# Performance work log

Hardware: AMD Instinct MI355X
Metric: run time of the kernel (lower is better)

The kernel has to match this reference:

```python
import jax, jax.numpy as jnp
import numpy as np

B, T, DM, DFE, DH, DRH = 32, 2048, 128, 64, 64, 64
E, NF, NSF, TOPK = 8, 16, 64, 2
LN_EPS = 1e-5


def setup_inputs() -> dict:
    key = jax.random.key(0)
    ks = jax.random.split(key, 18)
    s = 0.05
    # base expert i owns columns [16*i, 16*i+16); scale=2 -> expert e uses base e//2
    expert_idx = jnp.asarray(np.stack([np.arange(NF) + NF * (e // 2) for e in range(E)]), dtype=jnp.int32)  # [E,NF]
    stage_idx = jnp.arange(NSF, dtype=jnp.int32)  # stage uses all 64 columns
    return {
        'hidden': jax.random.normal(ks[0], (B, T, DM), jnp.float32),
        'feat': jax.random.normal(ks[1], (B, T, NSF), jnp.float32),
        'ln_g': jnp.ones((DM,), jnp.float32),
        'ln_b': jnp.zeros((DM,), jnp.float32),
        'Wp': jax.random.normal(ks[2], (NSF, DFE), jnp.float32) * s,
        'bp': jnp.zeros((DFE,), jnp.float32),
        'Wr1': jax.random.normal(ks[3], (DM + DFE, DRH), jnp.float32) * s,
        'br1': jnp.zeros((DRH,), jnp.float32),
        'Wr2': jax.random.normal(ks[4], (DRH, E), jnp.float32) * s,
        'br2': jnp.zeros((E,), jnp.float32),
        'Wf': jax.random.normal(ks[5], (E, NF, DFE), jnp.float32) * s,
        'bf': jnp.zeros((E, DFE), jnp.float32),
        'We1h': jax.random.normal(ks[6], (E, DM, DH), jnp.float32) * s,
        'We1f': jax.random.normal(ks[7], (E, DFE, DH), jnp.float32) * s,
        'be1': jnp.zeros((E, DH), jnp.float32),
        'We2': jax.random.normal(ks[8], (E, DH, DM), jnp.float32) * s,
        'be2': jnp.zeros((E, DM), jnp.float32),
        'alpha': jnp.asarray(1.0, jnp.float32),
        'item_seq_len': jax.random.randint(ks[9], (B,), 1, T + 1),
        'expert_idx': expert_idx,
        'stage_idx': stage_idx,
    }


def _layernorm(x, g, b):
    mu = jnp.mean(x, -1, keepdims=True)
    v = jnp.mean(jnp.square(x - mu), -1, keepdims=True)
    return (x - mu) * jax.lax.rsqrt(v + LN_EPS) * g + b


def reference(hidden, feat, ln_g, ln_b, Wp, bp, Wr1, br1, Wr2, br2,
              Wf, bf, We1h, We1f, be1, We2, be2, alpha,
              item_seq_len, expert_idx, stage_idx):
    h = _layernorm(hidden, ln_g, ln_b)                         # [B,T,DM]  pre_ln
    femb = feat[..., stage_idx] @ Wp + bp                      # [B,T,DFE] stage feature projection
    # --- token router: MLP -> softmax(temp=1) -> top-k renormalized gates ---
    rin = jnp.concatenate([h, femb], -1)                       # [B,T,DM+DFE]
    logits = jax.nn.relu(rin @ Wr1 + br1) @ Wr2 + br2          # [B,T,E]
    probs = jax.nn.softmax(logits, axis=-1)
    topv, topi = jax.lax.top_k(probs, TOPK)                    # [B,T,K]
    topv = topv / jnp.sum(topv, -1, keepdims=True)
    gates = jnp.sum(jax.nn.one_hot(topi, E, dtype=probs.dtype) * topv[..., None], axis=-2)  # [B,T,E]
    valid = jnp.arange(T)[None, :] < item_seq_len[:, None]     # [B,T]
    gates = gates * valid[..., None].astype(gates.dtype)
    # --- experts: per-expert feature gather + 2-layer GELU MLP (hidden + feat inputs) ---
    ef = feat[:, :, expert_idx]                                # [B,T,E,NF] gather
    x = jnp.einsum('btef,efd->bted', ef, Wf) + bf              # [B,T,E,DFE]
    h1 = jax.nn.gelu(jnp.einsum('btd,edo->bteo', h, We1h)
                     + jnp.einsum('bted,edo->bteo', x, We1f) + be1, approximate=False)
    eo = jnp.einsum('bteo,eod->bted', h1, We2) + be2           # [B,T,E,DM]
    moe = jnp.einsum('bte,bted->btd', gates, eo)               # weighted combine
    next_hidden = hidden + alpha * moe                         # residual, alpha_scale=1, dropout=0
    return next_hidden, gates, probs
```

## Files before the change

### kernel.cpp

```cpp
#include <hip/hip_runtime.h>
#include <hip/hip_bf16.h>


typedef unsigned short u16;
typedef __attribute__((ext_vector_type(8))) short bfrag;
typedef __attribute__((ext_vector_type(8))) u16 u16x8;
typedef __attribute__((ext_vector_type(4))) float facc;
typedef __attribute__((ext_vector_type(4))) float f32x4;

#define NTOK 65536
#define CAP 65536

#define OFF_CNT   ((size_t)0)
#define OFF_SEGM  ((size_t)256)
#define OFF_LTOK  ((size_t)512)
#define OFF_SMAPG (OFF_LTOK + (size_t)8*CAP*4)
#define OFF_HWS   (OFF_SMAPG + (size_t)NTOK*8)
#define OFF_EOTOK (OFF_HWS + (size_t)NTOK*128*2)
#define OFF_W1T   (OFF_EOTOK + (size_t)NTOK*2*128*2)
#define OFF_W2T   (OFF_W1T + 196608)
#define OFF_B1P   (OFF_W2T + 131072)
#define OFF_WPR   (OFF_B1P + 2048)
#define OFF_BR1P  (OFF_WPR + 16384)

__device__ __forceinline__ u16 f2bf(float f) {
  union { __hip_bfloat16 h; u16 u; } cv;
  cv.h = __float2bfloat16(f);
  return cv.u;
}
__device__ __forceinline__ float bf2f(u16 u) {
  return __uint_as_float(((unsigned)u) << 16);
}

__global__ __launch_bounds__(256)
void k0_pre(const float* __restrict__ Wp, const float* __restrict__ bp,
            const float* __restrict__ Wr1, const float* __restrict__ br1,
            const float* __restrict__ Wf, const float* __restrict__ bfv,
            const float* __restrict__ We1h, const float* __restrict__ We1f,
            const float* __restrict__ be1, const float* __restrict__ We2,
            float* __restrict__ Wpr, float* __restrict__ br1p,
            u16* __restrict__ w1t, u16* __restrict__ w2t, float* __restrict__ b1p)
{
  int j = blockIdx.x * 256 + threadIdx.x;
  if (j < 4096) {
    int i = j >> 6, o = j & 63;
    float s = 0.f;
    for (int k = 0; k < 64; ++k) s += Wp[i*64+k] * Wr1[(128+k)*64 + o];
    Wpr[i*64+o] = s;
  } else if (j < 4160) {
    int o = j - 4096;
    float s = br1[o];
    for (int k = 0; k < 64; ++k) s += bp[k] * Wr1[(128+k)*64 + o];
    br1p[o] = s;
  } else if (j < 4160 + 98304) {
    int idx = j - 4160;
    int e = idx / 12288; int rem = idx % 12288;
    int jj = rem / 192; int k = rem % 192;
    float v = 0.f;
    if (k < 128) v = We1h[(e*128 + k)*64 + jj];
    else if (k < 144) {
      int i = k - 128; float s = 0.f;
      for (int d = 0; d < 64; ++d) s += Wf[(e*16+i)*64 + d] * We1f[(e*64+d)*64 + jj];
      v = s;
    }
    size_t byte = (size_t)(e*64 + jj)*384 + ((2*k) ^ ((jj & 7) << 4));
    *(u16*)((char*)w1t + byte) = f2bf(v);
  } else if (j < 4160 + 98304 + 65536) {
    int idx = j - 4160 - 98304;
    int e = idx / 8192; int rem = idx % 8192;
    int d = rem / 64; int k = rem & 63;
    float v = We2[(e*64 + k)*128 + d];
    size_t byte = (size_t)(e*128 + d)*128 + ((2*k) ^ ((d & 7) << 4));
    *(u16*)((char*)w2t + byte) = f2bf(v);
  } else if (j < 4160 + 98304 + 65536 + 512) {
    int idx = j - 4160 - 98304 - 65536;
    int e = idx >> 6, o = idx & 63;
    float s = be1[e*64 + o];
    for (int d = 0; d < 64; ++d) s += bfv[e*64 + d] * We1f[(e*64+d)*64 + o];
    b1p[e*64 + o] = s;
  }
}

__global__ __launch_bounds__(256, 4)
void k1_router(const float* __restrict__ hidden, const float* __restrict__ feat,
               const float* __restrict__ ln_g, const float* __restrict__ ln_b,
               const float* __restrict__ Wr1, const float* __restrict__ Wr2,
               const float* __restrict__ br2, const int* __restrict__ seqlen,
               const int* __restrict__ sidx_g,
               const float* __restrict__ Wpr, const float* __restrict__ br1p,
               float* __restrict__ outG, float* __restrict__ outP,
               u16* __restrict__ hws, int* __restrict__ cnt,
               int* __restrict__ listTok, float* __restrict__ smapG)
{
  __shared__ float At[64*64];
  __shared__ float Wc[64*64];
  __shared__ float sW2[512];
  __shared__ float sb1[64], sg[128], sb[128], sbr2[8];
  __shared__ int ssidx[64];
  __shared__ int lcnt[8], lbase[8];
  __shared__ int ltok[8][64];
  __shared__ float tg[64][2];

  int tid = threadIdx.x;
  for (int i = tid; i < 512; i += 256) sW2[i] = Wr2[i];
  if (tid < 128) sg[tid] = ln_g[tid]; else sb[tid-128] = ln_b[tid-128];
  if (tid < 64) { sb1[tid] = br1p[tid]; ssidx[tid] = sidx_g[tid]; }
  if (tid >= 64 && tid < 72) sbr2[tid-64] = br2[tid-64];
  if (tid >= 72 && tid < 80) lcnt[tid-72] = 0;
  __syncthreads();

  int tok = tid >> 2, q = tid & 3;
  int t = blockIdx.x * 64 + tok;

  f32x4 x[8];
  #pragma unroll
  for (int i = 0; i < 8; ++i) x[i] = *(const f32x4*)(hidden + (size_t)t*128 + q*32 + i*4);
  float s = 0.f;
  #pragma unroll
  for (int i = 0; i < 8; ++i) { s += x[i][0] + x[i][1]; s += x[i][2] + x[i][3]; }
  s += __shfl_xor(s, 1, 64); s += __shfl_xor(s, 2, 64);
  float mu = s * (1.f/128.f);
  float v = 0.f;
  #pragma unroll
  for (int i = 0; i < 8; ++i) {
    #pragma unroll
    for (int j = 0; j < 4; ++j) { float d = x[i][j] - mu; v = fmaf(d, d, v); }
  }
  v += __shfl_xor(v, 1, 64); v += __shfl_xor(v, 2, 64);
  float rs = rsqrtf(v * (1.f/128.f) + 1e-5f);
  #pragma unroll
  for (int i = 0; i < 8; ++i) {
    #pragma unroll
    for (int j = 0; j < 4; ++j) {
      int c = q*32 + i*4 + j;
      x[i][j] = (x[i][j] - mu) * rs * sg[c] + sb[c];
    }
  }
  #pragma unroll
  for (int m = 0; m < 4; ++m) {
    u16x8 o;
    #pragma unroll
    for (int j = 0; j < 4; ++j) { o[j] = f2bf(x[2*m][j]); o[4+j] = f2bf(x[2*m+1][j]); }
    *(u16x8*)(hws + (size_t)t*128 + q*32 + m*8) = o;
  }
  float fv[16];
  #pragma unroll
  for (int i = 0; i < 16; ++i) fv[i] = feat[(size_t)t*64 + ssidx[q*16 + i]];

  float acc[4][4];
  #pragma unroll
  for (int i = 0; i < 4; ++i)
    #pragma unroll
    for (int p = 0; p < 4; ++p) acc[i][p] = 0.f;

  int tb = tid >> 4;
  int ob = (tid & 15) * 4;

  #pragma unroll 1
  for (int c = 0; c < 3; ++c) {
    __syncthreads();
    if (c < 2) {
      if ((c == 0) ? (q < 2) : (q >= 2)) {
        int kbase = (c == 0) ? q*32 : (q-2)*32;
        #pragma unroll
        for (int i = 0; i < 8; ++i)
          #pragma unroll
          for (int j = 0; j < 4; ++j) {
            int kr = kbase + i*4 + j;
            int byte = (kr << 8) + ((((tok >> 2) ^ ((kr >> 2) & 15)) << 4) | ((tok & 3) << 2));
            *(float*)((char*)At + byte) = x[i][j];
          }
      }
    } else {
      #pragma unroll
      for (int i = 0; i < 16; ++i) {
        int kr = q*16 + i;
        int byte = (kr << 8) + ((((tok >> 2) ^ ((kr >> 2) & 15)) << 4) | ((tok & 3) << 2));
        *(float*)((char*)At + byte) = fv[i];
      }
    }
    const float* wsrc = (c == 0) ? Wr1 : (c == 1) ? (Wr1 + 4096) : Wpr;
    for (int i = tid; i < 1024; i += 256) ((f32x4*)Wc)[i] = ((const f32x4*)wsrc)[i];
    __syncthreads();
    #pragma unroll 4
    for (int k = 0; k < 64; ++k) {
      f32x4 a4 = *(const f32x4*)((const char*)At + (k << 8) + ((tb ^ ((k >> 2) & 15)) << 4));
      f32x4 b4 = *(const f32x4*)(Wc + k*64 + ob);
      #pragma unroll
      for (int i = 0; i < 4; ++i)
        #pragma unroll
        for (int p = 0; p < 4; ++p)
          acc[i][p] = fmaf(a4[i], b4[p], acc[i][p]);
    }
  }

  float w2r[4][8];
  #pragma unroll
  for (int p = 0; p < 4; ++p)
    #pragma unroll
    for (int e = 0; e < 8; ++e) w2r[p][e] = sW2[(ob + p)*8 + e];
  float b1r[4];
  #pragma unroll
  for (int p = 0; p < 4; ++p) b1r[p] = sb1[ob + p];

  int j16 = tid & 15;
  #pragma unroll 1
  for (int ti = 0; ti < 4; ++ti) {
    float lo[8];
    #pragma unroll
    for (int e = 0; e < 8; ++e) lo[e] = 0.f;
    #pragma unroll
    for (int p = 0; p < 4; ++p) {
      float z = fmaxf(acc[ti][p] + b1r[p], 0.f);
      #pragma unroll
      for (int e = 0; e < 8; ++e) lo[e] = fmaf(z, w2r[p][e], lo[e]);
    }
    #pragma unroll
    for (int m = 1; m < 16; m <<= 1) {
      #pragma unroll
      for (int e = 0; e < 8; ++e) lo[e] += __shfl_xor(lo[e], m, 64);
    }
    #pragma unroll
    for (int e = 0; e < 8; ++e) lo[e] += sbr2[e];

    int tloc = tb*4 + ti;
    int tt = blockIdx.x*64 + tloc;
    float mx = lo[0];
    #pragma unroll
    for (int e = 1; e < 8; ++e) mx = fmaxf(mx, lo[e]);
    float ex[8]; float ss = 0.f;
    #pragma unroll
    for (int e = 0; e < 8; ++e) { ex[e] = __expf(lo[e] - mx); ss += ex[e]; }
    float inv = 1.f / ss;
    float p[8];
    #pragma unroll
    for (int e = 0; e < 8; ++e) p[e] = ex[e] * inv;
    float p1 = p[0]; int i1 = 0;
    #pragma unroll
    for (int e = 1; e < 8; ++e) { bool tk2 = p[e] > p1; p1 = tk2 ? p[e] : p1; i1 = tk2 ? e : i1; }
    float p2 = -1.f; int i2 = 0;
    #pragma unroll
    for (int e = 0; e < 8; ++e) { bool tk2 = (e != i1) && (p[e] > p2); p2 = tk2 ? p[e] : p2; i2 = tk2 ? e : i2; }
    bool valid = (tt & 2047) < seqlen[tt >> 11];
    float gden = 1.f / (p1 + p2);
    float g1 = p1 * gden, g2 = p2 * gden;
    float pv = p[0];
    #pragma unroll
    for (int e = 1; e < 8; ++e) pv = (j16 == e) ? p[e] : pv;
    if (j16 < 8) outP[(size_t)tt*8 + j16] = pv;
    float gv = (j16 == i1) ? g1 : ((j16 == i2) ? g2 : 0.f);
    if (!valid) gv = 0.f;
    if (j16 < 8) outG[(size_t)tt*8 + j16] = gv;
    if (j16 == 0) {
      if (valid) {
        int lp = atomicAdd(&lcnt[i1], 1); ltok[i1][lp] = (tt << 1);
        lp = atomicAdd(&lcnt[i2], 1);     ltok[i2][lp] = (tt << 1) | 1;
        tg[tloc][0] = g1; tg[tloc][1] = g2;
      } else {
        tg[tloc][0] = 0.f; tg[tloc][1] = 0.f;
      }
    }
  }

  __syncthreads();
  if (tid < 8) lbase[tid] = atomicAdd(&cnt[tid], lcnt[tid]);
  __syncthreads();
  #pragma unroll 1
  for (int e = 0; e < 8; ++e) {
    int ncnt = lcnt[e];
    if (tid < ncnt) listTok[(size_t)e*CAP + lbase[e] + tid] = ltok[e][tid];
  }
  if (tid < 64) {
    float2 g; g.x = tg[tid][0]; g.y = tg[tid][1];
    ((float2*)smapG)[blockIdx.x*64 + tid] = g;
  }
}

__global__ void k1b_prefix(const int* __restrict__ cnt, int* __restrict__ segm)
{
  if (threadIdx.x == 0 && blockIdx.x == 0) {
    int s = 0;
    #pragma unroll
    for (int e = 0; e < 8; ++e) { segm[e] = s; s += (cnt[e] + 63) >> 6; }
    segm[8] = s;
  }
}

__global__ __launch_bounds__(256)
void k2_experts(const float* __restrict__ feat, const u16* __restrict__ hws,
                const u16* __restrict__ w1t, const u16* __restrict__ w2t,
                const float* __restrict__ b1p, const float* __restrict__ be2,
                const int* __restrict__ eidx_g, const int* __restrict__ cnt,
                const int* __restrict__ segm, const int* __restrict__ listTok,
                u16* __restrict__ eoTok)
{
  __shared__ u16 Xs[64*192];
  __shared__ u16 W1s[64*192];
  __shared__ u16 W2s[128*64];
  __shared__ u16 H1s[64*64];
  __shared__ float b1s[64], be2s[128];
  __shared__ int sent[64];
  __shared__ int seidx[16];
  __shared__ int snr;

  int b = blockIdx.x;
  if (b >= segm[8]) return;
  int e = 0;
  #pragma unroll
  for (int i = 1; i < 8; ++i) if (b >= segm[i]) e = i;
  int row0 = (b - segm[e]) << 6;
  int n = cnt[e];
  int nr = n - row0; if (nr > 64) nr = 64;
  int tid = threadIdx.x;
  if (tid == 0) snr = nr;

  if (tid < 64) {
    int ent = 0;
    if (tid < nr) ent = listTok[(size_t)e*CAP + row0 + tid];
    sent[tid] = ent;
    b1s[tid] = b1p[e*64 + tid];
  }
  if (tid >= 64 && tid < 192) be2s[tid - 64] = be2[e*128 + tid - 64];
  if (tid >= 192 && tid < 208) seidx[tid-192] = eidx_g[e*16 + tid - 192];
  {
    const u16x8* s1 = (const u16x8*)(w1t + e*64*192);
    u16x8* d1 = (u16x8*)W1s;
    for (int i = tid; i < 1536; i += 256) d1[i] = s1[i];
    const u16x8* s2 = (const u16x8*)(w2t + e*128*64);
    u16x8* d2 = (u16x8*)W2s;
    for (int i = tid; i < 1024; i += 256) d2[i] = s2[i];
  }
  __syncthreads();
  for (int c = tid; c < 1024; c += 256) {
    int r = c >> 4, p = c & 15;
    u16x8 v = *(const u16x8*)(hws + (size_t)(sent[r] >> 1)*128 + p*8);
    *(u16x8*)((char*)Xs + r*384 + ((p*16) ^ ((r & 7) << 4))) = v;
  }
  if (tid < 128) {
    int r = tid >> 1, hf = tid & 1;
    int tk = sent[r] >> 1;
    u16x8 ov;
    #pragma unroll
    for (int p = 0; p < 8; ++p) ov[p] = f2bf(feat[(size_t)tk*64 + seidx[hf*8 + p]]);
    *(u16x8*)((char*)Xs + r*384 + ((256 + hf*16) ^ ((r & 7) << 4))) = ov;
    u16x8 zv = {0,0,0,0,0,0,0,0};
    *(u16x8*)((char*)Xs + r*384 + ((288 + hf*16) ^ ((r & 7) << 4))) = zv;
  }
  __syncthreads();

  int w = tid >> 6, lane = tid & 63;
  int la = lane & 15, lg = lane >> 4;
  int wm = (w >> 1) * 32, wn = (w & 1) * 32;

  facc acc[2][2];
  #pragma unroll
  for (int a = 0; a < 2; ++a)
    #pragma unroll
    for (int b2 = 0; b2 < 2; ++b2) { facc z = {0.f,0.f,0.f,0.f}; acc[a][b2] = z; }
  #pragma unroll
  for (int kc = 0; kc < 5; ++kc) {
    int kb = kc*64 + lg*16;
    bfrag af[2], bf2[2];
    #pragma unroll
    for (int mi = 0; mi < 2; ++mi) {
      int r = wm + mi*16 + la;
      af[mi] = *(const bfrag*)((const char*)Xs + r*384 + (kb ^ ((r & 7) << 4)));
    }
    #pragma unroll
    for (int ni = 0; ni < 2; ++ni) {
      int r = wn + ni*16 + la;
      bf2[ni] = *(const bfrag*)((const char*)W1s + r*384 + (kb ^ ((r & 7) << 4)));
    }
    #pragma unroll
    for (int mi = 0; mi < 2; ++mi)
      #pragma unroll
      for (int ni = 0; ni < 2; ++ni)
        acc[mi][ni] = __builtin_amdgcn_mfma_f32_16x16x32_bf16(af[mi], bf2[ni], acc[mi][ni], 0, 0, 0);
  }
  #pragma unroll
  for (int mi = 0; mi < 2; ++mi)
    #pragma unroll
    for (int ni = 0; ni < 2; ++ni)
      #pragma unroll
      for (int rg = 0; rg < 4; ++rg) {
        int r = wm + mi*16 + lg*4 + rg;
        int c = wn + ni*16 + la;
        float z = acc[mi][ni][rg] + b1s[c];
        float gl = 0.5f * z * (1.f + erff(z * 0.70710678118f));
        *(u16*)((char*)H1s + r*128 + ((2*c) ^ ((r & 7) << 4))) = f2bf(gl);
      }
  __syncthreads();

  facc acc2[2][4];
  #pragma unroll
  for (int a = 0; a < 2; ++a)
    #pragma unroll
    for (int b2 = 0; b2 < 4; ++b2) { facc z = {0.f,0.f,0.f,0.f}; acc2[a][b2] = z; }
  int wn2 = (w & 1) * 64;
  #pragma unroll
  for (int kc = 0; kc < 2; ++kc) {
    int kb = kc*64 + lg*16;
    bfrag af[2], bf2[4];
    #pragma unroll
    for (int mi = 0; mi < 2; ++mi) {
      int r = wm + mi*16 + la;
      af[mi] = *(const bfrag*)((const char*)H1s + r*128 + (kb ^ ((r & 7) << 4)));
    }
    #pragma unroll
    for (int ni = 0; ni < 4; ++ni) {
      int r = wn2 + ni*16 + la;
      bf2[ni] = *(const bfrag*)((const char*)W2s + r*128 + (kb ^ ((r & 7) << 4)));
    }
    #pragma unroll
    for (int mi = 0; mi < 2; ++mi)
      #pragma unroll
      for (int ni = 0; ni < 4; ++ni)
        acc2[mi][ni] = __builtin_amdgcn_mfma_f32_16x16x32_bf16(af[mi], bf2[ni], acc2[mi][ni], 0, 0, 0);
  }
  #pragma unroll
  for (int mi = 0; mi < 2; ++mi)
    #pragma unroll
    for (int ni = 0; ni < 4; ++ni)
      #pragma unroll
      for (int rg = 0; rg < 4; ++rg) {
        int r = wm + mi*16 + lg*4 + rg;
        int c = wn2 + ni*16 + la;
        if (r < snr) {
          float v = acc2[mi][ni][rg] + be2s[c];
          eoTok[(size_t)sent[r]*128 + c] = f2bf(v);
        }
      }
}

__global__ __launch_bounds__(256)
void k3_combine(const float* __restrict__ hidden, const float* __restrict__ smapG,
                const u16* __restrict__ eoTok, const float* __restrict__ alphap,
                float* __restrict__ outN)
{
  int tid = threadIdx.x;
  int tok = tid >> 2, q = tid & 3;
  int t = blockIdx.x*64 + tok;
  float2 g = ((const float2*)smapG)[t];
  float a = alphap[0];
  float ag0 = a * g.x, ag1 = a * g.y;
  const f32x4* hp = (const f32x4*)(hidden + (size_t)t*128 + q*32);
  f32x4* op = (f32x4*)(outN + (size_t)t*128 + q*32);
  const u16x8* e0 = (const u16x8*)(eoTok + ((size_t)t*2)*128 + q*32);
  const u16x8* e1 = (const u16x8*)(eoTok + ((size_t)t*2 + 1)*128 + q*32);
  #pragma unroll
  for (int i = 0; i < 4; ++i) {
    f32x4 r0 = hp[2*i], r1 = hp[2*i+1];
    if (g.x != 0.f) {
      u16x8 x0 = e0[i];
      #pragma unroll
      for (int j = 0; j < 4; ++j) { r0[j] = fmaf(ag0, bf2f(x0[j]), r0[j]); r1[j] = fmaf(ag0, bf2f(x0[4+j]), r1[j]); }
    }
    if (g.y != 0.f) {
      u16x8 x1 = e1[i];
      #pragma unroll
      for (int j = 0; j < 4; ++j) { r0[j] = fmaf(ag1, bf2f(x1[j]), r0[j]); r1[j] = fmaf(ag1, bf2f(x1[4+j]), r1[j]); }
    }
    op[2*i] = r0; op[2*i+1] = r1;
  }
}

extern "C" void kernel_launch(void* const* d_in, const int* in_sizes, int n_in,
                              void* d_out, int out_size, void* d_ws, size_t ws_size,
                              hipStream_t stream) {
  const float* hidden = (const float*)d_in[0];
  const float* feat   = (const float*)d_in[1];
  const float* ln_g   = (const float*)d_in[2];
  const float* ln_b   = (const float*)d_in[3];
  const float* Wp     = (const float*)d_in[4];
  const float* bp     = (const float*)d_in[5];
  const float* Wr1    = (const float*)d_in[6];
  const float* br1    = (const float*)d_in[7];
  const float* Wr2    = (const float*)d_in[8];
  const float* br2    = (const float*)d_in[9];
  const float* Wf     = (const float*)d_in[10];
  const float* bfv    = (const float*)d_in[11];
  const float* We1h   = (const float*)d_in[12];
  const float* We1f   = (const float*)d_in[13];
  const float* be1    = (const float*)d_in[14];
  const float* We2    = (const float*)d_in[15];
  const float* be2    = (const float*)d_in[16];
  const float* alpha  = (const float*)d_in[17];
  const int* seqlen   = (const int*)d_in[18];
  const int* eidx     = (const int*)d_in[19];
  const int* sidx     = (const int*)d_in[20];

  char* ws = (char*)d_ws;
  int*   cnt      = (int*)(ws + OFF_CNT);
  int*   segm     = (int*)(ws + OFF_SEGM);
  int*   listTok  = (int*)(ws + OFF_LTOK);
  float* smapG    = (float*)(ws + OFF_SMAPG);
  u16*   hws      = (u16*)(ws + OFF_HWS);
  u16*   eoTok    = (u16*)(ws + OFF_EOTOK);
  u16*   w1t      = (u16*)(ws + OFF_W1T);
  u16*   w2t      = (u16*)(ws + OFF_W2T);
  float* b1p      = (float*)(ws + OFF_B1P);
  float* Wpr      = (float*)(ws + OFF_WPR);
  float* br1p     = (float*)(ws + OFF_BR1P);

  float* outN = (float*)d_out;
  float* outG = outN + (size_t)NTOK * 128;
  float* outP = outG + (size_t)NTOK * 8;

  hipMemsetAsync(ws + OFF_CNT, 0, 256, stream);
  k0_pre<<<659, 256, 0, stream>>>(Wp, bp, Wr1, br1, Wf, bfv, We1h, We1f, be1, We2,
                                  Wpr, br1p, w1t, w2t, b1p);
  k1_router<<<1024, 256, 0, stream>>>(hidden, feat, ln_g, ln_b, Wr1, Wr2, br2, seqlen,
                                      sidx, Wpr, br1p, outG, outP, hws, cnt,
                                      listTok, smapG);
  k1b_prefix<<<1, 64, 0, stream>>>(cnt, segm);
  k2_experts<<<2056, 256, 0, stream>>>(feat, hws, w1t, w2t, b1p, be2, eidx,
                                       cnt, segm, listTok, eoTok);
  k3_combine<<<1024, 256, 0, stream>>>(hidden, smapG, eoTok, alpha, outN);
}
```

Baseline: 129.8 us.

## Drop prefix kernel, read expert weights from global, prefetch router weights

The separate single-thread prefix kernel is removed, and each expert block now computes its segment from the counts inline. The expert kernel stops staging the W1/W2 weights into shared memory. It reads MFMA B-fragments straight from global/L2, uses padded unswizzled LDS rows for X and H1, and gives each wave a 16-row M tile. The router kernel register-prefetches the next weight chunk while computing the current one and uses a different LDS swizzle. Together these cut one launch and LDS traffic and occupancy pressure, at the cost of more global/L2 weight reads per block.

```diff
diff --git a/kernel.cpp b/kernel.cpp
--- a/kernel.cpp
+++ b/kernel.cpp
@@ -12,13 +12,12 @@
 #define CAP 65536
 
 #define OFF_CNT   ((size_t)0)
-#define OFF_SEGM  ((size_t)256)
 #define OFF_LTOK  ((size_t)512)
 #define OFF_SMAPG (OFF_LTOK + (size_t)8*CAP*4)
 #define OFF_HWS   (OFF_SMAPG + (size_t)NTOK*8)
 #define OFF_EOTOK (OFF_HWS + (size_t)NTOK*128*2)
 #define OFF_W1T   (OFF_EOTOK + (size_t)NTOK*2*128*2)
-#define OFF_W2T   (OFF_W1T + 196608)
+#define OFF_W2T   (OFF_W1T + 163840)
 #define OFF_B1P   (OFF_W2T + 131072)
 #define OFF_WPR   (OFF_B1P + 2048)
 #define OFF_BR1P  (OFF_WPR + 16384)
@@ -52,10 +51,10 @@
     float s = br1[o];
     for (int k = 0; k < 64; ++k) s += bp[k] * Wr1[(128+k)*64 + o];
     br1p[o] = s;
-  } else if (j < 4160 + 98304) {
+  } else if (j < 4160 + 81920) {
     int idx = j - 4160;
-    int e = idx / 12288; int rem = idx % 12288;
-    int jj = rem / 192; int k = rem % 192;
+    int e = idx / 10240; int rem = idx % 10240;
+    int jj = rem / 160; int k = rem % 160;
     float v = 0.f;
     if (k < 128) v = We1h[(e*128 + k)*64 + jj];
     else if (k < 144) {
@@ -63,17 +62,14 @@
       for (int d = 0; d < 64; ++d) s += Wf[(e*16+i)*64 + d] * We1f[(e*64+d)*64 + jj];
       v = s;
     }
-    size_t byte = (size_t)(e*64 + jj)*384 + ((2*k) ^ ((jj & 7) << 4));
-    *(u16*)((char*)w1t + byte) = f2bf(v);
-  } else if (j < 4160 + 98304 + 65536) {
-    int idx = j - 4160 - 98304;
+    w1t[(size_t)(e*64 + jj)*160 + k] = f2bf(v);
+  } else if (j < 4160 + 81920 + 65536) {
+    int idx = j - 4160 - 81920;
     int e = idx / 8192; int rem = idx % 8192;
     int d = rem / 64; int k = rem & 63;
-    float v = We2[(e*64 + k)*128 + d];
-    size_t byte = (size_t)(e*128 + d)*128 + ((2*k) ^ ((d & 7) << 4));
-    *(u16*)((char*)w2t + byte) = f2bf(v);
-  } else if (j < 4160 + 98304 + 65536 + 512) {
-    int idx = j - 4160 - 98304 - 65536;
+    w2t[(size_t)(e*128 + d)*64 + k] = f2bf(We2[(e*64 + k)*128 + d]);
+  } else if (j < 4160 + 81920 + 65536 + 512) {
+    int idx = j - 4160 - 81920 - 65536;
     int e = idx >> 6, o = idx & 63;
     float s = be1[e*64 + o];
     for (int d = 0; d < 64; ++d) s += bfv[e*64 + d] * We1f[(e*64+d)*64 + o];
@@ -102,6 +98,11 @@
   __shared__ float tg[64][2];
 
   int tid = threadIdx.x;
+
+  f32x4 wpf[4];
+  #pragma unroll
+  for (int u = 0; u < 4; ++u) wpf[u] = ((const f32x4*)Wr1)[u*256 + tid];
+
   for (int i = tid; i < 512; i += 256) sW2[i] = Wr2[i];
   if (tid < 128) sg[tid] = ln_g[tid]; else sb[tid-128] = ln_b[tid-128];
   if (tid < 64) { sb1[tid] = br1p[tid]; ssidx[tid] = sidx_g[tid]; }
@@ -158,7 +159,6 @@
 
   #pragma unroll 1
   for (int c = 0; c < 3; ++c) {
-    __syncthreads();
     if (c < 2) {
       if ((c == 0) ? (q < 2) : (q >= 2)) {
         int kbase = (c == 0) ? q*32 : (q-2)*32;
@@ -167,24 +167,30 @@
           #pragma unroll
           for (int j = 0; j < 4; ++j) {
             int kr = kbase + i*4 + j;
-            int byte = (kr << 8) + ((((tok >> 2) ^ ((kr >> 2) & 15)) << 4) | ((tok & 3) << 2));
-            *(float*)((char*)At + byte) = x[i][j];
+            int slot = ((tok >> 2) ^ (kr & 15) ^ (kr >> 4)) & 15;
+            *(float*)((char*)At + (kr << 8) + (slot << 4) + ((tok & 3) << 2)) = x[i][j];
           }
       }
     } else {
       #pragma unroll
       for (int i = 0; i < 16; ++i) {
         int kr = q*16 + i;
-        int byte = (kr << 8) + ((((tok >> 2) ^ ((kr >> 2) & 15)) << 4) | ((tok & 3) << 2));
-        *(float*)((char*)At + byte) = fv[i];
+        int slot = ((tok >> 2) ^ (kr & 15) ^ (kr >> 4)) & 15;
+        *(float*)((char*)At + (kr << 8) + (slot << 4) + ((tok & 3) << 2)) = fv[i];
       }
     }
-    const float* wsrc = (c == 0) ? Wr1 : (c == 1) ? (Wr1 + 4096) : Wpr;
-    for (int i = tid; i < 1024; i += 256) ((f32x4*)Wc)[i] = ((const f32x4*)wsrc)[i];
+    #pragma unroll
+    for (int u = 0; u < 4; ++u) ((f32x4*)Wc)[u*256 + tid] = wpf[u];
     __syncthreads();
+    if (c < 2) {
+      const f32x4* nsrc = (c == 0) ? (const f32x4*)(Wr1 + 4096) : (const f32x4*)Wpr;
+      #pragma unroll
+      for (int u = 0; u < 4; ++u) wpf[u] = nsrc[u*256 + tid];
+    }
     #pragma unroll 4
     for (int k = 0; k < 64; ++k) {
-      f32x4 a4 = *(const f32x4*)((const char*)At + (k << 8) + ((tb ^ ((k >> 2) & 15)) << 4));
+      int slot = (tb ^ (k & 15) ^ (k >> 4)) & 15;
+      f32x4 a4 = *(const f32x4*)((const char*)At + (k << 8) + (slot << 4));
       f32x4 b4 = *(const f32x4*)(Wc + k*64 + ob);
       #pragma unroll
       for (int i = 0; i < 4; ++i)
@@ -192,6 +198,7 @@
         for (int p = 0; p < 4; ++p)
           acc[i][p] = fmaf(a4[i], b4[p], acc[i][p]);
     }
+    __syncthreads();
   }
 
   float w2r[4][8];
@@ -276,65 +283,47 @@
   }
 }
 
-__global__ void k1b_prefix(const int* __restrict__ cnt, int* __restrict__ segm)
-{
-  if (threadIdx.x == 0 && blockIdx.x == 0) {
-    int s = 0;
-    #pragma unroll
-    for (int e = 0; e < 8; ++e) { segm[e] = s; s += (cnt[e] + 63) >> 6; }
-    segm[8] = s;
-  }
-}
-
 __global__ __launch_bounds__(256)
 void k2_experts(const float* __restrict__ feat, const u16* __restrict__ hws,
                 const u16* __restrict__ w1t, const u16* __restrict__ w2t,
                 const float* __restrict__ b1p, const float* __restrict__ be2,
                 const int* __restrict__ eidx_g, const int* __restrict__ cnt,
-                const int* __restrict__ segm, const int* __restrict__ listTok,
-                u16* __restrict__ eoTok)
+                const int* __restrict__ listTok, u16* __restrict__ eoTok)
 {
-  __shared__ u16 Xs[64*192];
-  __shared__ u16 W1s[64*192];
-  __shared__ u16 W2s[128*64];
-  __shared__ u16 H1s[64*64];
+  __shared__ u16 Xs[64*168];
+  __shared__ u16 H1s[64*88];
   __shared__ float b1s[64], be2s[128];
   __shared__ int sent[64];
   __shared__ int seidx[16];
   __shared__ int snr;
 
-  int b = blockIdx.x;
-  if (b >= segm[8]) return;
-  int e = 0;
-  #pragma unroll
-  for (int i = 1; i < 8; ++i) if (b >= segm[i]) e = i;
-  int row0 = (b - segm[e]) << 6;
-  int n = cnt[e];
+  int b = blockIdx.x, tid = threadIdx.x;
+  int e = -1, row0 = 0, n = 0, accb = 0;
+  #pragma unroll
+  for (int i = 0; i < 8; ++i) {
+    int ci = cnt[i]; int ns = (ci + 63) >> 6;
+    if (e < 0 && b < accb + ns) { e = i; row0 = (b - accb) << 6; n = ci; }
+    accb += ns;
+  }
+  if (e < 0) return;
   int nr = n - row0; if (nr > 64) nr = 64;
-  int tid = threadIdx.x;
   if (tid == 0) snr = nr;
 
   if (tid < 64) {
-    int ent = 0;
-    if (tid < nr) ent = listTok[(size_t)e*CAP + row0 + tid];
+    int ent = (tid < nr) ? listTok[(size_t)e*CAP + row0 + tid] : 0;
     sent[tid] = ent;
     b1s[tid] = b1p[e*64 + tid];
-  }
-  if (tid >= 64 && tid < 192) be2s[tid - 64] = be2[e*128 + tid - 64];
-  if (tid >= 192 && tid < 208) seidx[tid-192] = eidx_g[e*16 + tid - 192];
-  {
-    const u16x8* s1 = (const u16x8*)(w1t + e*64*192);
-    u16x8* d1 = (u16x8*)W1s;
-    for (int i = tid; i < 1536; i += 256) d1[i] = s1[i];
-    const u16x8* s2 = (const u16x8*)(w2t + e*128*64);
-    u16x8* d2 = (u16x8*)W2s;
-    for (int i = tid; i < 1024; i += 256) d2[i] = s2[i];
-  }
-  __syncthreads();
-  for (int c = tid; c < 1024; c += 256) {
-    int r = c >> 4, p = c & 15;
-    u16x8 v = *(const u16x8*)(hws + (size_t)(sent[r] >> 1)*128 + p*8);
-    *(u16x8*)((char*)Xs + r*384 + ((p*16) ^ ((r & 7) << 4))) = v;
+  } else if (tid < 192) {
+    be2s[tid - 64] = be2[e*128 + tid - 64];
+  } else if (tid < 208) {
+    seidx[tid-192] = eidx_g[e*16 + tid - 192];
+  }
+  __syncthreads();
+
+  for (int c2 = tid; c2 < 1024; c2 += 256) {
+    int r = c2 >> 4, p = c2 & 15;
+    u16x8 vv = *(const u16x8*)(hws + (size_t)(sent[r] >> 1)*128 + p*8);
+    *(u16x8*)((char*)Xs + r*336 + p*16) = vv;
   }
   if (tid < 128) {
     int r = tid >> 1, hf = tid & 1;
@@ -342,94 +331,66 @@
     u16x8 ov;
     #pragma unroll
     for (int p = 0; p < 8; ++p) ov[p] = f2bf(feat[(size_t)tk*64 + seidx[hf*8 + p]]);
-    *(u16x8*)((char*)Xs + r*384 + ((256 + hf*16) ^ ((r & 7) << 4))) = ov;
+    *(u16x8*)((char*)Xs + r*336 + 256 + hf*16) = ov;
     u16x8 zv = {0,0,0,0,0,0,0,0};
-    *(u16x8*)((char*)Xs + r*384 + ((288 + hf*16) ^ ((r & 7) << 4))) = zv;
+    *(u16x8*)((char*)Xs + r*336 + 288 + hf*16) = zv;
   }
   __syncthreads();
 
   int w = tid >> 6, lane = tid & 63;
   int la = lane & 15, lg = lane >> 4;
-  int wm = (w >> 1) * 32, wn = (w & 1) * 32;
-
-  facc acc[2][2];
-  #pragma unroll
-  for (int a = 0; a < 2; ++a)
-    #pragma unroll
-    for (int b2 = 0; b2 < 2; ++b2) { facc z = {0.f,0.f,0.f,0.f}; acc[a][b2] = z; }
+  const u16* w1e = w1t + (size_t)e*64*160;
+  const u16* w2e = w2t + (size_t)e*128*64;
+
+  facc acc[4];
+  #pragma unroll
+  for (int ni = 0; ni < 4; ++ni) { facc z = {0.f,0.f,0.f,0.f}; acc[ni] = z; }
   #pragma unroll
   for (int kc = 0; kc < 5; ++kc) {
-    int kb = kc*64 + lg*16;
-    bfrag af[2], bf2[2];
-    #pragma unroll
-    for (int mi = 0; mi < 2; ++mi) {
-      int r = wm + mi*16 + la;
-      af[mi] = *(const bfrag*)((const char*)Xs + r*384 + (kb ^ ((r & 7) << 4)));
-    }
-    #pragma unroll
-    for (int ni = 0; ni < 2; ++ni) {
-      int r = wn + ni*16 + la;
-      bf2[ni] = *(const bfrag*)((const char*)W1s + r*384 + (kb ^ ((r & 7) << 4)));
-    }
-    #pragma unroll
-    for (int mi = 0; mi < 2; ++mi)
-      #pragma unroll
-      for (int ni = 0; ni < 2; ++ni)
-        acc[mi][ni] = __builtin_amdgcn_mfma_f32_16x16x32_bf16(af[mi], bf2[ni], acc[mi][ni], 0, 0, 0);
-  }
-  #pragma unroll
-  for (int mi = 0; mi < 2; ++mi)
-    #pragma unroll
-    for (int ni = 0; ni < 2; ++ni)
-      #pragma unroll
-      for (int rg = 0; rg < 4; ++rg) {
-        int r = wm + mi*16 + lg*4 + rg;
-        int c = wn + ni*16 + la;
-        float z = acc[mi][ni][rg] + b1s[c];
-        float gl = 0.5f * z * (1.f + erff(z * 0.70710678118f));
-        *(u16*)((char*)H1s + r*128 + ((2*c) ^ ((r & 7) << 4))) = f2bf(gl);
+    int r = w*16 + la;
+    bfrag af = *(const bfrag*)((const char*)Xs + r*336 + kc*64 + lg*16);
+    #pragma unroll
+    for (int ni = 0; ni < 4; ++ni) {
+      bfrag bf2 = *(const bfrag*)(w1e + (size_t)(ni*16 + la)*160 + kc*32 + lg*8);
+      acc[ni] = __builtin_amdgcn_mfma_f32_16x16x32_bf16(af, bf2, acc[ni], 0, 0, 0);
+    }
+  }
+  #pragma unroll
+  for (int ni = 0; ni < 4; ++ni)
+    #pragma unroll
+    for (int rg = 0; rg < 4; ++rg) {
+      int r = w*16 + lg*4 + rg;
+      int c = ni*16 + la;
+      float z = acc[ni][rg] + b1s[c];
+      float gl = 0.5f * z * (1.f + erff(z * 0.70710678118f));
+      *(u16*)((char*)H1s + r*176 + c*2) = f2bf(gl);
+    }
+  __syncthreads();
+
+  facc acc2[8];
+  #pragma unroll
+  for (int ni = 0; ni < 8; ++ni) { facc z = {0.f,0.f,0.f,0.f}; acc2[ni] = z; }
+  #pragma unroll
+  for (int kc = 0; kc < 2; ++kc) {
+    int r = w*16 + la;
+    bfrag af = *(const bfrag*)((const char*)H1s + r*176 + kc*64 + lg*16);
+    #pragma unroll
+    for (int ni = 0; ni < 8; ++ni) {
+      bfrag bf2 = *(const bfrag*)(w2e + (size_t)(ni*16 + la)*64 + kc*32 + lg*8);
+      acc2[ni] = __builtin_amdgcn_mfma_f32_16x16x32_bf16(af, bf2, acc2[ni], 0, 0, 0);
+    }
+  }
+  #pragma unroll
+  for (int ni = 0; ni < 8; ++ni)
+    #pragma unroll
+    for (int rg = 0; rg < 4; ++rg) {
+      int r = w*16 + lg*4 + rg;
+      int c = ni*16 + la;
+      if (r < snr) {
+        float vv = acc2[ni][rg] + be2s[c];
+        eoTok[(size_t)sent[r]*128 + c] = f2bf(vv);
       }
-  __syncthreads();
-
-  facc acc2[2][4];
-  #pragma unroll
-  for (int a = 0; a < 2; ++a)
-    #pragma unroll
-    for (int b2 = 0; b2 < 4; ++b2) { facc z = {0.f,0.f,0.f,0.f}; acc2[a][b2] = z; }
-  int wn2 = (w & 1) * 64;
-  #pragma unroll
-  for (int kc = 0; kc < 2; ++kc) {
-    int kb = kc*64 + lg*16;
-    bfrag af[2], bf2[4];
-    #pragma unroll
-    for (int mi = 0; mi < 2; ++mi) {
-      int r = wm + mi*16 + la;
-      af[mi] = *(const bfrag*)((const char*)H1s + r*128 + (kb ^ ((r & 7) << 4)));
-    }
-    #pragma unroll
-    for (int ni = 0; ni < 4; ++ni) {
-      int r = wn2 + ni*16 + la;
-      bf2[ni] = *(const bfrag*)((const char*)W2s + r*128 + (kb ^ ((r & 7) << 4)));
-    }
-    #pragma unroll
-    for (int mi = 0; mi < 2; ++mi)
-      #pragma unroll
-      for (int ni = 0; ni < 4; ++ni)
-        acc2[mi][ni] = __builtin_amdgcn_mfma_f32_16x16x32_bf16(af[mi], bf2[ni], acc2[mi][ni], 0, 0, 0);
-  }
-  #pragma unroll
-  for (int mi = 0; mi < 2; ++mi)
-    #pragma unroll
-    for (int ni = 0; ni < 4; ++ni)
-      #pragma unroll
-      for (int rg = 0; rg < 4; ++rg) {
-        int r = wm + mi*16 + lg*4 + rg;
-        int c = wn2 + ni*16 + la;
-        if (r < snr) {
-          float v = acc2[mi][ni][rg] + be2s[c];
-          eoTok[(size_t)sent[r]*128 + c] = f2bf(v);
-        }
-      }
+    }
 }
 
 __global__ __launch_bounds__(256)
@@ -491,7 +452,6 @@
 
   char* ws = (char*)d_ws;
   int*   cnt      = (int*)(ws + OFF_CNT);
-  int*   segm     = (int*)(ws + OFF_SEGM);
   int*   listTok  = (int*)(ws + OFF_LTOK);
   float* smapG    = (float*)(ws + OFF_SMAPG);
   u16*   hws      = (u16*)(ws + OFF_HWS);
@@ -507,13 +467,12 @@
   float* outP = outG + (size_t)NTOK * 8;
 
   hipMemsetAsync(ws + OFF_CNT, 0, 256, stream);
-  k0_pre<<<659, 256, 0, stream>>>(Wp, bp, Wr1, br1, Wf, bfv, We1h, We1f, be1, We2,
+  k0_pre<<<595, 256, 0, stream>>>(Wp, bp, Wr1, br1, Wf, bfv, We1h, We1f, be1, We2,
                                   Wpr, br1p, w1t, w2t, b1p);
   k1_router<<<1024, 256, 0, stream>>>(hidden, feat, ln_g, ln_b, Wr1, Wr2, br2, seqlen,
                                       sidx, Wpr, br1p, outG, outP, hws, cnt,
                                       listTok, smapG);
-  k1b_prefix<<<1, 64, 0, stream>>>(cnt, segm);
   k2_experts<<<2056, 256, 0, stream>>>(feat, hws, w1t, w2t, b1p, be2, eidx,
-                                       cnt, segm, listTok, eoTok);
+                                       cnt, listTok, eoTok);
   k3_combine<<<1024, 256, 0, stream>>>(hidden, smapG, eoTok, alpha, outN);
 }
```

Measured after the change: 131.6 us. Within noise of the previous version (+1.4%).
